# Kernel optimization log

Hardware: AMD Instinct MI355X
Metric: run time of the kernel (lower is better)

The kernel has to match this reference:

```python
import jax, jax.numpy as jnp
import numpy as np

N = 100000
E = 1600000
G = 128


def _degrees(src, dst, n):
    ones = jnp.ones(src.shape[0], dtype=jnp.float32)
    deg_out = jax.ops.segment_sum(ones, src, num_segments=n)
    deg_in = jax.ops.segment_sum(ones, dst, num_segments=n)
    return jnp.maximum(deg_out, 1.0), jnp.maximum(deg_in, 1.0)


def gcn_conv(x, W, b, src, dst, norm_out, norm_in):
    # DGL GraphConv, norm='both': scale src by d_out^-1/2, sum over edges,
    # scale dst by d_in^-1/2, then linear. Weight applied first (out<=in) --
    # mathematically identical, cheaper gather.
    h = (x * norm_out[:, None]) @ W          # [N, out]
    m = h[src]                               # [E, out] gather
    agg = jax.ops.segment_sum(m, dst, num_segments=N)  # [N, out] scatter-add
    return agg * norm_in[:, None] + b


def setup_inputs() -> dict:
    key = jax.random.key(0)
    ks = jax.random.split(key, 8)
    x = jax.random.normal(ks[0], (N, 128), dtype=jnp.float32)
    W1 = jax.random.normal(ks[1], (128, 64), dtype=jnp.float32) * (1.0 / np.sqrt(128))
    b1 = jnp.zeros((64,), dtype=jnp.float32)
    W2 = jax.random.normal(ks[2], (64, 16), dtype=jnp.float32) * (1.0 / np.sqrt(64))
    b2 = jnp.zeros((16,), dtype=jnp.float32)
    src = jax.random.randint(ks[3], (E,), 0, N, dtype=jnp.int32)
    dst = jax.random.randint(ks[4], (E,), 0, N, dtype=jnp.int32)
    graph_ids = jnp.sort(jax.random.randint(ks[5], (N,), 0, G, dtype=jnp.int32))
    return {"x": x, "W1": W1, "b1": b1, "W2": W2, "b2": b2,
            "src": src, "dst": dst, "graph_ids": graph_ids}


def reference(x, W1, b1, W2, b2, src, dst, graph_ids):
    deg_out, deg_in = _degrees(src, dst, N)
    norm_out = jax.lax.rsqrt(deg_out)
    norm_in = jax.lax.rsqrt(deg_in)
    h = gcn_conv(x, W1, b1, src, dst, norm_out, norm_in)
    h = jax.nn.relu(h)
    # dropout(p=0.2) is identity in eval mode
    h = gcn_conv(h, W2, b2, src, dst, norm_out, norm_in)
    # dgl.mean_nodes: per-graph mean pooling
    sums = jax.ops.segment_sum(h, graph_ids, num_segments=G)      # [G, 16]
    counts = jax.ops.segment_sum(jnp.ones((N,), jnp.float32), graph_ids, num_segments=G)
    return sums / jnp.maximum(counts, 1.0)[:, None]
```

## Files before the change

kernel.cpp:

```cpp
#include <hip/hip_runtime.h>
#include <hip/hip_fp16.h>

#define N_NODES 100000
#define N_EDGES 1600000
#define N_GRAPHS 128
#define NBUCK 391
#define NBLK 512
#define NE4 (N_EDGES / 4)
#define CHUNK_E4 782
#define LDX 136

typedef unsigned long long u64;
typedef unsigned int u32;
typedef unsigned char u8;
typedef _Float16 f16;
typedef f16 half8 __attribute__((ext_vector_type(8)));
typedef f16 half4v __attribute__((ext_vector_type(4)));
typedef float floatx4 __attribute__((ext_vector_type(4)));

__global__ __launch_bounds__(256) void k_cnt(const int4* __restrict__ src4,
                                             const int4* __restrict__ dst4,
                                             int* __restrict__ counts_d,
                                             int* __restrict__ counts_s) {
  __shared__ int hd[NBUCK], hs[NBUCK];
  const int t = threadIdx.x, blk = blockIdx.x;
  for (int j = t; j < NBUCK; j += 256) { hd[j] = 0; hs[j] = 0; }
  __syncthreads();
  const int start = blk * CHUNK_E4;
  const int end = min(start + CHUNK_E4, NE4);
  for (int i = start + t; i < end; i += 256) {
    int4 d = dst4[i]; int4 s = src4[i];
    atomicAdd(&hd[d.x >> 8], 1); atomicAdd(&hd[d.y >> 8], 1);
    atomicAdd(&hd[d.z >> 8], 1); atomicAdd(&hd[d.w >> 8], 1);
    atomicAdd(&hs[s.x >> 8], 1); atomicAdd(&hs[s.y >> 8], 1);
    atomicAdd(&hs[s.z >> 8], 1); atomicAdd(&hs[s.w >> 8], 1);
  }
  __syncthreads();
  for (int j = t; j < NBUCK; j += 256) {
    counts_d[j * NBLK + blk] = hd[j];
    counts_s[j * NBLK + blk] = hs[j];
  }
}

__global__ __launch_bounds__(512) void k_scanA(int* __restrict__ counts_d,
                                               int* __restrict__ counts_s,
                                               int* __restrict__ totals_d,
                                               int* __restrict__ totals_s) {
  __shared__ int s[512];
  const int b = blockIdx.x, t = threadIdx.x;
  int v = counts_d[b * NBLK + t];
  s[t] = v;
  __syncthreads();
  for (int off = 1; off < 512; off <<= 1) {
    int a = (t >= off) ? s[t - off] : 0;
    __syncthreads(); s[t] += a; __syncthreads();
  }
  counts_d[b * NBLK + t] = s[t] - v;
  if (t == 511) totals_d[b] = s[t];
  __syncthreads();
  v = counts_s[b * NBLK + t];
  s[t] = v;
  __syncthreads();
  for (int off = 1; off < 512; off <<= 1) {
    int a = (t >= off) ? s[t - off] : 0;
    __syncthreads(); s[t] += a; __syncthreads();
  }
  counts_s[b * NBLK + t] = s[t] - v;
  if (t == 511) totals_s[b] = s[t];
}

__global__ __launch_bounds__(512) void k_scanB(const int* __restrict__ totals_d,
                                               const int* __restrict__ totals_s,
                                               int* __restrict__ boff_d,
                                               int* __restrict__ boff_s,
                                               int* __restrict__ row_ptr) {
  __shared__ int s[512];
  const int t = threadIdx.x;
  int v = (t < NBUCK) ? totals_d[t] : 0;
  s[t] = v;
  __syncthreads();
  for (int off = 1; off < 512; off <<= 1) {
    int a = (t >= off) ? s[t - off] : 0;
    __syncthreads(); s[t] += a; __syncthreads();
  }
  if (t < NBUCK) boff_d[t] = s[t] - v;
  if (t == 0) { boff_d[NBUCK] = N_EDGES; row_ptr[N_NODES] = N_EDGES; }
  __syncthreads();
  v = (t < NBUCK) ? totals_s[t] : 0;
  s[t] = v;
  __syncthreads();
  for (int off = 1; off < 512; off <<= 1) {
    int a = (t >= off) ? s[t - off] : 0;
    __syncthreads(); s[t] += a; __syncthreads();
  }
  if (t < NBUCK) boff_s[t] = s[t] - v;
  if (t == 0) boff_s[NBUCK] = N_EDGES;
}

__global__ __launch_bounds__(256) void k_scatter(const int4* __restrict__ src4,
                                                 const int4* __restrict__ dst4,
                                                 const int* __restrict__ counts_d,
                                                 const int* __restrict__ counts_s,
                                                 const int* __restrict__ boff_d,
                                                 const int* __restrict__ boff_s,
                                                 u32* __restrict__ ed,
                                                 u8* __restrict__ ssk8) {
  __shared__ int cur_d[NBUCK], cur_s[NBUCK];
  const int t = threadIdx.x, blk = blockIdx.x;
  for (int j = t; j < NBUCK; j += 256) {
    cur_d[j] = boff_d[j] + counts_d[j * NBLK + blk];
    cur_s[j] = boff_s[j] + counts_s[j * NBLK + blk];
  }
  __syncthreads();
  const int start = blk * CHUNK_E4;
  const int end = min(start + CHUNK_E4, NE4);
  for (int i = start + t; i < end; i += 256) {
    int4 d4 = dst4[i]; int4 s4 = src4[i];
    {
      int d = d4.x, s = s4.x;
      int pd = atomicAdd(&cur_d[d >> 8], 1);
      ed[pd] = ((u32)(d & 255) << 24) | (u32)s;
      int ps = atomicAdd(&cur_s[s >> 8], 1);
      ssk8[ps] = (u8)(s & 255);
    }
    {
      int d = d4.y, s = s4.y;
      int pd = atomicAdd(&cur_d[d >> 8], 1);
      ed[pd] = ((u32)(d & 255) << 24) | (u32)s;
      int ps = atomicAdd(&cur_s[s >> 8], 1);
      ssk8[ps] = (u8)(s & 255);
    }
    {
      int d = d4.z, s = s4.z;
      int pd = atomicAdd(&cur_d[d >> 8], 1);
      ed[pd] = ((u32)(d & 255) << 24) | (u32)s;
      int ps = atomicAdd(&cur_s[s >> 8], 1);
      ssk8[ps] = (u8)(s & 255);
    }
    {
      int d = d4.w, s = s4.w;
      int pd = atomicAdd(&cur_d[d >> 8], 1);
      ed[pd] = ((u32)(d & 255) << 24) | (u32)s;
      int ps = atomicAdd(&cur_s[s >> 8], 1);
      ssk8[ps] = (u8)(s & 255);
    }
  }
}

__global__ __launch_bounds__(256) void k_bucket_csr(const u32* __restrict__ ed,
                                                    const int* __restrict__ boff_d,
                                                    const u8* __restrict__ ssk8,
                                                    const int* __restrict__ boff_s,
                                                    int* __restrict__ row_ptr,
                                                    float* __restrict__ norm_in,
                                                    float* __restrict__ norm_out,
                                                    int* __restrict__ edge_src) {
  __shared__ int hist[256], scanbuf[256], cursor[256], hist2[256];
  const int b = blockIdx.x, t = threadIdx.x;
  const int base = b << 8;
  hist[t] = 0; hist2[t] = 0;
  __syncthreads();
  const int slo = boff_s[b], shi = boff_s[b + 1];
  for (int i = slo + t; i < shi; i += 256)
    atomicAdd(&hist2[ssk8[i]], 1);
  const int lo = boff_d[b], hi = boff_d[b + 1];
  for (int i = lo + t; i < hi; i += 256)
    atomicAdd(&hist[ed[i] >> 24], 1);
  __syncthreads();
  int node = base + t;
  if (node < N_NODES)
    norm_out[node] = rsqrtf(fmaxf((float)hist2[t], 1.0f));
  int v = hist[t];
  scanbuf[t] = v;
  __syncthreads();
  for (int off = 1; off < 256; off <<= 1) {
    int a = (t >= off) ? scanbuf[t - off] : 0;
    __syncthreads(); scanbuf[t] += a; __syncthreads();
  }
  int excl = scanbuf[t] - v;
  if (node < N_NODES) {
    row_ptr[node] = lo + excl;
    norm_in[node] = rsqrtf(fmaxf((float)v, 1.0f));
  }
  cursor[t] = excl;
  __syncthreads();
  for (int i = lo + t; i < hi; i += 256) {
    u32 e = ed[i];
    int p = atomicAdd(&cursor[e >> 24], 1);
    edge_src[lo + p] = (int)(e & 0x00FFFFFFu);
  }
}

__global__ __launch_bounds__(256) void k_gemm1(const float* __restrict__ x,
                                               const float* __restrict__ W1,
                                               const float* __restrict__ norm_out,
                                               __half* __restrict__ h1h) {
  __shared__ __align__(16) f16 Xs[64 * LDX];
  __shared__ __align__(16) f16 Ws[64 * LDX];
  const int t = threadIdx.x;
  const int row0 = blockIdx.x * 64;

  const float4* W4 = (const float4*)W1;
  for (int i = t; i < 2048; i += 256) {
    int k = i >> 4, n4 = (i & 15) * 4;
    float4 v = W4[i];
    Ws[(n4 + 0) * LDX + k] = (f16)v.x;
    Ws[(n4 + 1) * LDX + k] = (f16)v.y;
    Ws[(n4 + 2) * LDX + k] = (f16)v.z;
    Ws[(n4 + 3) * LDX + k] = (f16)v.w;
  }
  const float4* x4 = (const float4*)x;
  #pragma unroll
  for (int i = 0; i < 8; ++i) {
    int idx = t + 256 * i;
    int r = idx >> 5, c4 = idx & 31;
    int row = row0 + r;
    float4 v = make_float4(0.f, 0.f, 0.f, 0.f);
    if (row < N_NODES) {
      float s = norm_out[row];
      v = x4[(size_t)row * 32 + c4];
      v.x *= s; v.y *= s; v.z *= s; v.w *= s;
    }
    half4v h = { (f16)v.x, (f16)v.y, (f16)v.z, (f16)v.w };
    *(half4v*)&Xs[r * LDX + c4 * 4] = h;
  }
  __syncthreads();

  const int w = t >> 6, l = t & 63;
  const int m = l & 15, quad = l >> 4;
  floatx4 c0 = {0.f,0.f,0.f,0.f}, c1 = {0.f,0.f,0.f,0.f};
  floatx4 c2 = {0.f,0.f,0.f,0.f}, c3 = {0.f,0.f,0.f,0.f};
  const f16* xrow = &Xs[(w * 16 + m) * LDX + quad * 8];
  const f16* wrow = &Ws[m * LDX + quad * 8];
  #pragma unroll
  for (int kb = 0; kb < 4; ++kb) {
    half8 a  = *(const half8*)(xrow + kb * 32);
    half8 b0 = *(const half8*)(wrow + kb * 32);
    half8 b1 = *(const half8*)(wrow + 16 * LDX + kb * 32);
    half8 b2 = *(const half8*)(wrow + 32 * LDX + kb * 32);
    half8 b3 = *(const half8*)(wrow + 48 * LDX + kb * 32);
    c0 = __builtin_amdgcn_mfma_f32_16x16x32_f16(a, b0, c0, 0, 0, 0);
    c1 = __builtin_amdgcn_mfma_f32_16x16x32_f16(a, b1, c1, 0, 0, 0);
    c2 = __builtin_amdgcn_mfma_f32_16x16x32_f16(a, b2, c2, 0, 0, 0);
    c3 = __builtin_amdgcn_mfma_f32_16x16x32_f16(a, b3, c3, 0, 0, 0);
  }
  #pragma unroll
  for (int r = 0; r < 4; ++r) {
    int row = row0 + w * 16 + quad * 4 + r;
    if (row < N_NODES + 1) {
      __half* dst = h1h + (size_t)row * 64 + m;
      dst[0]  = __float2half(c0[r]);
      dst[16] = __float2half(c1[r]);
      dst[32] = __float2half(c2[r]);
      dst[48] = __float2half(c3[r]);
    }
  }
}

__global__ __launch_bounds__(256) void k_gather_l1(const int* __restrict__ row_ptr,
                                                   const int* __restrict__ edge_src,
                                                   const __half* __restrict__ h1h,
                                                   const float* __restrict__ norm_in,
                                                   const float* __restrict__ norm_out,
                                                   const float* __restrict__ b1,
                                                   const float* __restrict__ W2,
                                                   __half* __restrict__ h2h) {
  __shared__ float W2s[64 * 17];
  const int t = threadIdx.x;
  for (int i = t; i < 64 * 16; i += 256) W2s[(i >> 4) * 17 + (i & 15)] = W2[i];
  if (blockIdx.x == 0 && t < 16) h2h[(size_t)N_NODES * 16 + t] = __float2half(0.f);
  __syncthreads();

  const int w = t >> 6;
  const int l = t & 63;
  const int n = blockIdx.x * 4 + w;
  const int p = l >> 3;
  const u32 c = (u32)(l & 7);

  const uint4* __restrict__ h1q = (const uint4*)h1h;
  const int lo = row_ptr[n], hi = row_ptr[n + 1];

  float2 f0 = {0.f,0.f}, f1 = {0.f,0.f}, f2 = {0.f,0.f}, f3 = {0.f,0.f};
  for (int i = lo; i < hi; i += 16) {
    int idx = i + (l & 15);
    int sv = (idx < hi) ? edge_src[idx] : (int)N_NODES;
    int sa = __shfl(sv, p, 64);
    int sb = __shfl(sv, p + 8, 64);
    uint4 va = h1q[(u32)sa * 8u + c];
    uint4 vb = h1q[(u32)sb * 8u + c];
    float2 g;
    g = __half22float2(*(__half2*)&va.x); f0.x += g.x; f0.y += g.y;
    g = __half22float2(*(__half2*)&va.y); f1.x += g.x; f1.y += g.y;
    g = __half22float2(*(__half2*)&va.z); f2.x += g.x; f2.y += g.y;
    g = __half22float2(*(__half2*)&va.w); f3.x += g.x; f3.y += g.y;
    g = __half22float2(*(__half2*)&vb.x); f0.x += g.x; f0.y += g.y;
    g = __half22float2(*(__half2*)&vb.y); f1.x += g.x; f1.y += g.y;
    g = __half22float2(*(__half2*)&vb.z); f2.x += g.x; f2.y += g.y;
    g = __half22float2(*(__half2*)&vb.w); f3.x += g.x; f3.y += g.y;
  }
  float hr[8] = { f0.x, f0.y, f1.x, f1.y, f2.x, f2.y, f3.x, f3.y };
  #pragma unroll
  for (int e = 0; e < 8; ++e) {
    hr[e] += __shfl_xor(hr[e], 8, 64);
    hr[e] += __shfl_xor(hr[e], 16, 64);
    hr[e] += __shfl_xor(hr[e], 32, 64);
  }
  const float ni = norm_in[n];
  const float4 bA = ((const float4*)b1)[c * 2];
  const float4 bB = ((const float4*)b1)[c * 2 + 1];
  hr[0] = fmaxf(hr[0] * ni + bA.x, 0.f);
  hr[1] = fmaxf(hr[1] * ni + bA.y, 0.f);
  hr[2] = fmaxf(hr[2] * ni + bA.z, 0.f);
  hr[3] = fmaxf(hr[3] * ni + bA.w, 0.f);
  hr[4] = fmaxf(hr[4] * ni + bB.x, 0.f);
  hr[5] = fmaxf(hr[5] * ni + bB.y, 0.f);
  hr[6] = fmaxf(hr[6] * ni + bB.z, 0.f);
  hr[7] = fmaxf(hr[7] * ni + bB.w, 0.f);

  const int j = l & 15, p2 = l >> 4;
  float partial = 0.f;
  #pragma unroll
  for (int e = 0; e < 8; ++e) {
    float v0 = __shfl(hr[e], p2 * 2, 64);
    float v1 = __shfl(hr[e], p2 * 2 + 1, 64);
    partial += v0 * W2s[(p2 * 16 + e) * 17 + j];
    partial += v1 * W2s[(p2 * 16 + 8 + e) * 17 + j];
  }
  partial += __shfl_xor(partial, 16, 64);
  partial += __shfl_xor(partial, 32, 64);
  if (l < 16) h2h[(size_t)n * 16 + l] = __float2half(norm_out[n] * partial);
}

__global__ __launch_bounds__(256) void k_gather_l2(const int* __restrict__ row_ptr,
                                                   const int* __restrict__ edge_src,
                                                   const __half* __restrict__ h2h,
                                                   const float* __restrict__ norm_in,
                                                   float* __restrict__ agg2) {
  const int t = threadIdx.x;
  const int w = t >> 6;
  const int l = t & 63;
  const int n = blockIdx.x * 4 + w;
  const int f2 = l & 7;
  const int p = l >> 3;

  const u32* __restrict__ h2u = (const u32*)h2h;
  const int lo = row_ptr[n], hi = row_ptr[n + 1];

  float ax = 0.f, ay = 0.f, bx = 0.f, by = 0.f;
  for (int base = lo; base < hi; base += 16) {
    int i1 = base + p, i2 = base + p + 8;
    int s0 = (i1 < hi) ? edge_src[i1] : (int)N_NODES;
    int s1 = (i2 < hi) ? edge_src[i2] : (int)N_NODES;
    u32 v0 = h2u[(u32)s0 * 8u + (u32)f2];
    u32 v1 = h2u[(u32)s1 * 8u + (u32)f2];
    float2 g0 = __half22float2(*(__half2*)&v0);
    float2 g1 = __half22float2(*(__half2*)&v1);
    ax += g0.x; ay += g0.y;
    bx += g1.x; by += g1.y;
  }
  float sx = ax + bx, sy = ay + by;
  sx += __shfl_xor(sx, 8, 64);  sy += __shfl_xor(sy, 8, 64);
  sx += __shfl_xor(sx, 16, 64); sy += __shfl_xor(sy, 16, 64);
  sx += __shfl_xor(sx, 32, 64); sy += __shfl_xor(sy, 32, 64);
  if (l < 8) {
    float ni = norm_in[n];
    ((float2*)agg2)[(size_t)n * 8 + f2] = make_float2(sx * ni, sy * ni);
  }
}

__global__ __launch_bounds__(256) void k_pool(const float* __restrict__ agg2,
                                              const float* __restrict__ b2,
                                              const int* __restrict__ gid,
                                              float* __restrict__ out) {
  const int g = blockIdx.x;
  __shared__ int s_lo, s_hi;
  if (threadIdx.x == 0) {
    int a = 0, b = N_NODES;
    while (a < b) { int m = (a + b) >> 1; if (gid[m] < g) a = m + 1; else b = m; }
    s_lo = a;
    b = N_NODES;
    while (a < b) { int m = (a + b) >> 1; if (gid[m] < g + 1) a = m + 1; else b = m; }
    s_hi = a;
  }
  __syncthreads();
  const int lo = s_lo, hi = s_hi, cnt = hi - lo;
  const int j = threadIdx.x & 15;
  const int r = threadIdx.x >> 4;
  float acc = 0.f;
  for (int n = lo + r; n < hi; n += 16)
    acc += agg2[(size_t)n * 16 + j];

  __shared__ float red[256];
  red[threadIdx.x] = acc;
  __syncthreads();
  #pragma unroll
  for (int s = 8; s > 0; s >>= 1) {
    if (r < s) red[threadIdx.x] += red[threadIdx.x + s * 16];
    __syncthreads();
  }
  if (r == 0)
    out[g * 16 + j] = (cnt > 0) ? (red[j] / (float)cnt + b2[j]) : 0.0f;
}

extern "C" void kernel_launch(void* const* d_in, const int* in_sizes, int n_in,
                              void* d_out, int out_size, void* d_ws, size_t ws_size,
                              hipStream_t stream) {
  const float* x   = (const float*)d_in[0];
  const float* W1  = (const float*)d_in[1];
  const float* b1  = (const float*)d_in[2];
  const float* W2  = (const float*)d_in[3];
  const float* b2  = (const float*)d_in[4];
  const int*   src = (const int*)d_in[5];
  const int*   dst = (const int*)d_in[6];
  const int*   gid = (const int*)d_in[7];
  float* out = (float*)d_out;

  const size_t N = N_NODES, E = N_EDGES;
  float* wsf = (float*)d_ws;
  int*   wsi = (int*)d_ws;

  float* norm_out = wsf;
  float* norm_in  = wsf + N;
  int*   row_ptr  = wsi + 2 * N;
  int*   edge_src = wsi + 3 * N + 16;
  size_t S = 3 * N + 16 + E;
  u8*    ssk8     = (u8*)(wsi + S);
  int*   counts_d = wsi + S + 400000;
  int*   counts_s = wsi + S + 600192;
  int*   totals_d = wsi + S + 800384;
  int*   totals_s = wsi + S + 800776;
  int*   boff_d   = wsi + S + 801168;
  int*   boff_s   = wsi + S + 801560;
  u32*   ed       = (u32*)(wsi + S + 801952);
  __half* h1h     = (__half*)(wsi + S);
  __half* h2h     = (__half*)(wsi + S + 32 * N + 32);
  float*  agg2    = (float*)(wsi + S + 40 * N + 40);

  const int4* src4 = (const int4*)src;
  const int4* dst4 = (const int4*)dst;

  k_cnt       <<<NBLK, 256, 0, stream>>>(src4, dst4, counts_d, counts_s);
  k_scanA     <<<NBUCK, 512, 0, stream>>>(counts_d, counts_s, totals_d, totals_s);
  k_scanB     <<<1, 512, 0, stream>>>(totals_d, totals_s, boff_d, boff_s, row_ptr);
  k_scatter   <<<NBLK, 256, 0, stream>>>(src4, dst4, counts_d, counts_s, boff_d, boff_s, ed, ssk8);
  k_bucket_csr<<<NBUCK, 256, 0, stream>>>(ed, boff_d, ssk8, boff_s, row_ptr, norm_in, norm_out, edge_src);
  k_gemm1     <<<(N_NODES + 64) / 64, 256, 0, stream>>>(x, W1, norm_out, h1h);
  k_gather_l1 <<<N_NODES / 4, 256, 0, stream>>>(row_ptr, edge_src, h1h, norm_in, norm_out, b1, W2, h2h);
  k_gather_l2 <<<N_NODES / 4, 256, 0, stream>>>(row_ptr, edge_src, h2h, norm_in, agg2);
  k_pool      <<<N_GRAPHS, 256, 0, stream>>>(agg2, b2, gid, out);
}
```

Measured before the change: 295.2 us.

## Replace per-node CSR with two-pass bucket sort and shared-memory atomic aggregation

The per-node CSR build is replaced by a two-pass radix-style sort: edges are first bucketed by source (for locality), then by destination into buckets of 64 nodes. The gather kernels now process one 64-node bucket per block and accumulate features with shared-memory float atomics instead of computing per-node row pointers. The two scans merge their second level via a last-block flag, which drops a launch. This aims to cut the cost of building the CSR and improve gather locality, but it adds heavy LDS atomic traffic and an extra pass over 8-byte edge records.

Measured after the change: 1.028 ms. 3.48x slower.

```diff
diff --git a/kernel.cpp b/kernel.cpp
--- a/kernel.cpp
+++ b/kernel.cpp
@@ -4,10 +4,12 @@
 #define N_NODES 100000
 #define N_EDGES 1600000
 #define N_GRAPHS 128
-#define NBUCK 391
+#define SB 391
+#define DB 1563
 #define NBLK 512
 #define NE4 (N_EDGES / 4)
-#define CHUNK_E4 782
+#define CH4 782
+#define CH64 3125
 #define LDX 136
 
 typedef unsigned long long u64;
@@ -18,176 +20,184 @@
 typedef f16 half4v __attribute__((ext_vector_type(4)));
 typedef float floatx4 __attribute__((ext_vector_type(4)));
 
-__global__ __launch_bounds__(256) void k_cnt(const int4* __restrict__ src4,
-                                             const int4* __restrict__ dst4,
-                                             int* __restrict__ counts_d,
-                                             int* __restrict__ counts_s) {
-  __shared__ int hd[NBUCK], hs[NBUCK];
-  const int t = threadIdx.x, blk = blockIdx.x;
-  for (int j = t; j < NBUCK; j += 256) { hd[j] = 0; hs[j] = 0; }
-  __syncthreads();
-  const int start = blk * CHUNK_E4;
-  const int end = min(start + CHUNK_E4, NE4);
+__global__ __launch_bounds__(256) void k_cnt_s(const int4* __restrict__ src4,
+                                               int* __restrict__ cs, int* __restrict__ flags) {
+  __shared__ int h[SB];
+  const int t = threadIdx.x, b = blockIdx.x;
+  if (b == 0 && t < 16) flags[t] = 0;
+  for (int j = t; j < SB; j += 256) h[j] = 0;
+  __syncthreads();
+  const int start = b * CH4, end = min(start + CH4, NE4);
   for (int i = start + t; i < end; i += 256) {
-    int4 d = dst4[i]; int4 s = src4[i];
-    atomicAdd(&hd[d.x >> 8], 1); atomicAdd(&hd[d.y >> 8], 1);
-    atomicAdd(&hd[d.z >> 8], 1); atomicAdd(&hd[d.w >> 8], 1);
-    atomicAdd(&hs[s.x >> 8], 1); atomicAdd(&hs[s.y >> 8], 1);
-    atomicAdd(&hs[s.z >> 8], 1); atomicAdd(&hs[s.w >> 8], 1);
-  }
-  __syncthreads();
-  for (int j = t; j < NBUCK; j += 256) {
-    counts_d[j * NBLK + blk] = hd[j];
-    counts_s[j * NBLK + blk] = hs[j];
-  }
-}
-
-__global__ __launch_bounds__(512) void k_scanA(int* __restrict__ counts_d,
-                                               int* __restrict__ counts_s,
-                                               int* __restrict__ totals_d,
-                                               int* __restrict__ totals_s) {
+    int4 s = src4[i];
+    atomicAdd(&h[s.x >> 8], 1); atomicAdd(&h[s.y >> 8], 1);
+    atomicAdd(&h[s.z >> 8], 1); atomicAdd(&h[s.w >> 8], 1);
+  }
+  __syncthreads();
+  for (int j = t; j < SB; j += 256) cs[j * NBLK + b] = h[j];
+}
+
+__global__ __launch_bounds__(512) void k_scan_s(int* __restrict__ cs, int* __restrict__ ts,
+                                                int* __restrict__ boff_s, int* __restrict__ flags) {
   __shared__ int s[512];
+  __shared__ int lastflag;
   const int b = blockIdx.x, t = threadIdx.x;
-  int v = counts_d[b * NBLK + t];
+  int v = cs[b * NBLK + t];
   s[t] = v;
   __syncthreads();
-  for (int off = 1; off < 512; off <<= 1) {
-    int a = (t >= off) ? s[t - off] : 0;
+  for (int o = 1; o < 512; o <<= 1) {
+    int a = (t >= o) ? s[t - o] : 0;
     __syncthreads(); s[t] += a; __syncthreads();
   }
-  counts_d[b * NBLK + t] = s[t] - v;
-  if (t == 511) totals_d[b] = s[t];
-  __syncthreads();
-  v = counts_s[b * NBLK + t];
+  cs[b * NBLK + t] = s[t] - v;
+  if (t == 511) atomicExch(&ts[b], s[t]);
+  if (t == 0) { __threadfence(); lastflag = (atomicAdd(&flags[0], 1) == SB - 1); }
+  __syncthreads();
+  if (!lastflag) return;
+  int v2 = (t < SB) ? atomicAdd(&ts[t], 0) : 0;
+  s[t] = v2;
+  __syncthreads();
+  for (int o = 1; o < 512; o <<= 1) {
+    int a = (t >= o) ? s[t - o] : 0;
+    __syncthreads(); s[t] += a; __syncthreads();
+  }
+  if (t <= SB) boff_s[t] = s[t] - v2;
+}
+
+__global__ __launch_bounds__(256) void k_scatter_s(const int4* __restrict__ src4,
+                                                   const int4* __restrict__ dst4,
+                                                   const int* __restrict__ cs,
+                                                   const int* __restrict__ boff_s,
+                                                   u64* __restrict__ ed_s, u8* __restrict__ ssk8) {
+  __shared__ int cur[SB];
+  const int t = threadIdx.x, b = blockIdx.x;
+  for (int j = t; j < SB; j += 256) cur[j] = boff_s[j] + cs[j * NBLK + b];
+  __syncthreads();
+  const int start = b * CH4, end = min(start + CH4, NE4);
+  for (int i = start + t; i < end; i += 256) {
+    int4 s4 = src4[i]; int4 d4 = dst4[i];
+    {
+      int s = s4.x, d = d4.x;
+      int ps = atomicAdd(&cur[s >> 8], 1);
+      ed_s[ps] = ((u64)(u32)d << 32) | (u32)s;
+      ssk8[ps] = (u8)(s & 255);
+    }
+    {
+      int s = s4.y, d = d4.y;
+      int ps = atomicAdd(&cur[s >> 8], 1);
+      ed_s[ps] = ((u64)(u32)d << 32) | (u32)s;
+      ssk8[ps] = (u8)(s & 255);
+    }
+    {
+      int s = s4.z, d = d4.z;
+      int ps = atomicAdd(&cur[s >> 8], 1);
+      ed_s[ps] = ((u64)(u32)d << 32) | (u32)s;
+      ssk8[ps] = (u8)(s & 255);
+    }
+    {
+      int s = s4.w, d = d4.w;
+      int ps = atomicAdd(&cur[s >> 8], 1);
+      ed_s[ps] = ((u64)(u32)d << 32) | (u32)s;
+      ssk8[ps] = (u8)(s & 255);
+    }
+  }
+}
+
+__global__ __launch_bounds__(256) void k_cnt_d(const u64* __restrict__ ed_s,
+                                               int* __restrict__ cd) {
+  __shared__ int h[DB];
+  const int t = threadIdx.x, b = blockIdx.x;
+  for (int j = t; j < DB; j += 256) h[j] = 0;
+  __syncthreads();
+  const int start = b * CH64, end = start + CH64;
+  for (int i = start + t; i < end; i += 256) {
+    u32 d = (u32)(ed_s[i] >> 32);
+    atomicAdd(&h[d >> 6], 1);
+  }
+  __syncthreads();
+  for (int j = t; j < DB; j += 256) cd[j * NBLK + b] = h[j];
+}
+
+__global__ __launch_bounds__(512) void k_scan_d(int* __restrict__ cd, int* __restrict__ td,
+                                                int* __restrict__ boff_d, int* __restrict__ flags) {
+  __shared__ int s[512];
+  __shared__ int lastflag;
+  const int b = blockIdx.x, t = threadIdx.x;
+  int v = cd[b * NBLK + t];
   s[t] = v;
   __syncthreads();
-  for (int off = 1; off < 512; off <<= 1) {
-    int a = (t >= off) ? s[t - off] : 0;
+  for (int o = 1; o < 512; o <<= 1) {
+    int a = (t >= o) ? s[t - o] : 0;
     __syncthreads(); s[t] += a; __syncthreads();
   }
-  counts_s[b * NBLK + t] = s[t] - v;
-  if (t == 511) totals_s[b] = s[t];
-}
-
-__global__ __launch_bounds__(512) void k_scanB(const int* __restrict__ totals_d,
-                                               const int* __restrict__ totals_s,
-                                               int* __restrict__ boff_d,
-                                               int* __restrict__ boff_s,
-                                               int* __restrict__ row_ptr) {
-  __shared__ int s[512];
-  const int t = threadIdx.x;
-  int v = (t < NBUCK) ? totals_d[t] : 0;
-  s[t] = v;
-  __syncthreads();
-  for (int off = 1; off < 512; off <<= 1) {
-    int a = (t >= off) ? s[t - off] : 0;
+  cd[b * NBLK + t] = s[t] - v;
+  if (t == 511) atomicExch(&td[b], s[t]);
+  if (t == 0) { __threadfence(); lastflag = (atomicAdd(&flags[1], 1) == DB - 1); }
+  __syncthreads();
+  if (!lastflag) return;
+  const int g = t * 4;
+  int v0 = (g + 0 < DB) ? atomicAdd(&td[g + 0], 0) : 0;
+  int v1 = (g + 1 < DB) ? atomicAdd(&td[g + 1], 0) : 0;
+  int v2 = (g + 2 < DB) ? atomicAdd(&td[g + 2], 0) : 0;
+  int v3 = (g + 3 < DB) ? atomicAdd(&td[g + 3], 0) : 0;
+  int tsum = v0 + v1 + v2 + v3;
+  s[t] = tsum;
+  __syncthreads();
+  for (int o = 1; o < 512; o <<= 1) {
+    int a = (t >= o) ? s[t - o] : 0;
     __syncthreads(); s[t] += a; __syncthreads();
   }
-  if (t < NBUCK) boff_d[t] = s[t] - v;
-  if (t == 0) { boff_d[NBUCK] = N_EDGES; row_ptr[N_NODES] = N_EDGES; }
-  __syncthreads();
-  v = (t < NBUCK) ? totals_s[t] : 0;
-  s[t] = v;
-  __syncthreads();
-  for (int off = 1; off < 512; off <<= 1) {
-    int a = (t >= off) ? s[t - off] : 0;
-    __syncthreads(); s[t] += a; __syncthreads();
-  }
-  if (t < NBUCK) boff_s[t] = s[t] - v;
-  if (t == 0) boff_s[NBUCK] = N_EDGES;
-}
-
-__global__ __launch_bounds__(256) void k_scatter(const int4* __restrict__ src4,
-                                                 const int4* __restrict__ dst4,
-                                                 const int* __restrict__ counts_d,
-                                                 const int* __restrict__ counts_s,
-                                                 const int* __restrict__ boff_d,
-                                                 const int* __restrict__ boff_s,
-                                                 u32* __restrict__ ed,
-                                                 u8* __restrict__ ssk8) {
-  __shared__ int cur_d[NBUCK], cur_s[NBUCK];
-  const int t = threadIdx.x, blk = blockIdx.x;
-  for (int j = t; j < NBUCK; j += 256) {
-    cur_d[j] = boff_d[j] + counts_d[j * NBLK + blk];
-    cur_s[j] = boff_s[j] + counts_s[j * NBLK + blk];
-  }
-  __syncthreads();
-  const int start = blk * CHUNK_E4;
-  const int end = min(start + CHUNK_E4, NE4);
+  int excl = s[t] - tsum;
+  if (g + 0 <= DB) boff_d[g + 0] = excl;
+  if (g + 1 <= DB) boff_d[g + 1] = excl + v0;
+  if (g + 2 <= DB) boff_d[g + 2] = excl + v0 + v1;
+  if (g + 3 <= DB) boff_d[g + 3] = excl + v0 + v1 + v2;
+}
+
+__global__ __launch_bounds__(256) void k_scatter_d(const u64* __restrict__ ed_s,
+                                                   const int* __restrict__ cd,
+                                                   const int* __restrict__ boff_d,
+                                                   u32* __restrict__ ed_d) {
+  __shared__ int cur[DB];
+  const int t = threadIdx.x, b = blockIdx.x;
+  for (int j = t; j < DB; j += 256) cur[j] = boff_d[j] + cd[j * NBLK + b];
+  __syncthreads();
+  const int start = b * CH64, end = start + CH64;
   for (int i = start + t; i < end; i += 256) {
-    int4 d4 = dst4[i]; int4 s4 = src4[i];
-    {
-      int d = d4.x, s = s4.x;
-      int pd = atomicAdd(&cur_d[d >> 8], 1);
-      ed[pd] = ((u32)(d & 255) << 24) | (u32)s;
-      int ps = atomicAdd(&cur_s[s >> 8], 1);
-      ssk8[ps] = (u8)(s & 255);
-    }
-    {
-      int d = d4.y, s = s4.y;
-      int pd = atomicAdd(&cur_d[d >> 8], 1);
-      ed[pd] = ((u32)(d & 255) << 24) | (u32)s;
-      int ps = atomicAdd(&cur_s[s >> 8], 1);
-      ssk8[ps] = (u8)(s & 255);
-    }
-    {
-      int d = d4.z, s = s4.z;
-      int pd = atomicAdd(&cur_d[d >> 8], 1);
-      ed[pd] = ((u32)(d & 255) << 24) | (u32)s;
-      int ps = atomicAdd(&cur_s[s >> 8], 1);
-      ssk8[ps] = (u8)(s & 255);
-    }
-    {
-      int d = d4.w, s = s4.w;
-      int pd = atomicAdd(&cur_d[d >> 8], 1);
-      ed[pd] = ((u32)(d & 255) << 24) | (u32)s;
-      int ps = atomicAdd(&cur_s[s >> 8], 1);
-      ssk8[ps] = (u8)(s & 255);
-    }
-  }
-}
-
-__global__ __launch_bounds__(256) void k_bucket_csr(const u32* __restrict__ ed,
-                                                    const int* __restrict__ boff_d,
-                                                    const u8* __restrict__ ssk8,
-                                                    const int* __restrict__ boff_s,
-                                                    int* __restrict__ row_ptr,
-                                                    float* __restrict__ norm_in,
-                                                    float* __restrict__ norm_out,
-                                                    int* __restrict__ edge_src) {
-  __shared__ int hist[256], scanbuf[256], cursor[256], hist2[256];
+    u64 e = ed_s[i];
+    u32 d = (u32)(e >> 32), s = (u32)e;
+    int pd = atomicAdd(&cur[d >> 6], 1);
+    ed_d[pd] = ((d & 63u) << 26) | s;
+  }
+}
+
+__global__ __launch_bounds__(256) void k_norms(const u8* __restrict__ ssk8,
+                                               const int* __restrict__ boff_s,
+                                               const u32* __restrict__ ed_d,
+                                               const int* __restrict__ boff_d,
+                                               float* __restrict__ norm_out,
+                                               float* __restrict__ norm_in) {
+  __shared__ int h[256];
   const int b = blockIdx.x, t = threadIdx.x;
-  const int base = b << 8;
-  hist[t] = 0; hist2[t] = 0;
-  __syncthreads();
-  const int slo = boff_s[b], shi = boff_s[b + 1];
-  for (int i = slo + t; i < shi; i += 256)
-    atomicAdd(&hist2[ssk8[i]], 1);
-  const int lo = boff_d[b], hi = boff_d[b + 1];
-  for (int i = lo + t; i < hi; i += 256)
-    atomicAdd(&hist[ed[i] >> 24], 1);
-  __syncthreads();
-  int node = base + t;
-  if (node < N_NODES)
-    norm_out[node] = rsqrtf(fmaxf((float)hist2[t], 1.0f));
-  int v = hist[t];
-  scanbuf[t] = v;
-  __syncthreads();
-  for (int off = 1; off < 256; off <<= 1) {
-    int a = (t >= off) ? scanbuf[t - off] : 0;
-    __syncthreads(); scanbuf[t] += a; __syncthreads();
-  }
-  int excl = scanbuf[t] - v;
-  if (node < N_NODES) {
-    row_ptr[node] = lo + excl;
-    norm_in[node] = rsqrtf(fmaxf((float)v, 1.0f));
-  }
-  cursor[t] = excl;
-  __syncthreads();
-  for (int i = lo + t; i < hi; i += 256) {
-    u32 e = ed[i];
-    int p = atomicAdd(&cursor[e >> 24], 1);
-    edge_src[lo + p] = (int)(e & 0x00FFFFFFu);
+  if (b < SB) {
+    h[t] = 0;
+    __syncthreads();
+    const int lo = boff_s[b], hi = boff_s[b + 1];
+    for (int i = lo + t; i < hi; i += 256) atomicAdd(&h[ssk8[i]], 1);
+    __syncthreads();
+    int node = (b << 8) + t;
+    if (node < N_NODES) norm_out[node] = rsqrtf(fmaxf((float)h[t], 1.0f));
+  } else {
+    const int bb = b - SB;
+    if (t < 64) h[t] = 0;
+    __syncthreads();
+    const int lo = boff_d[bb], hi = boff_d[bb + 1];
+    for (int i = lo + t; i < hi; i += 256) atomicAdd(&h[ed_d[i] >> 26], 1);
+    __syncthreads();
+    if (t < 64) {
+      int node = (bb << 6) + t;
+      if (node < N_NODES) norm_in[node] = rsqrtf(fmaxf((float)h[t], 1.0f));
+    }
   }
 }
 
@@ -257,114 +267,117 @@
   }
 }
 
-__global__ __launch_bounds__(256) void k_gather_l1(const int* __restrict__ row_ptr,
-                                                   const int* __restrict__ edge_src,
+__global__ __launch_bounds__(256) void k_gather_l1(const int* __restrict__ boff_d,
+                                                   const u32* __restrict__ ed_d,
                                                    const __half* __restrict__ h1h,
                                                    const float* __restrict__ norm_in,
                                                    const float* __restrict__ norm_out,
                                                    const float* __restrict__ b1,
                                                    const float* __restrict__ W2,
                                                    __half* __restrict__ h2h) {
-  __shared__ float W2s[64 * 17];
-  const int t = threadIdx.x;
-  for (int i = t; i < 64 * 16; i += 256) W2s[(i >> 4) * 17 + (i & 15)] = W2[i];
-  if (blockIdx.x == 0 && t < 16) h2h[(size_t)N_NODES * 16 + t] = __float2half(0.f);
-  __syncthreads();
-
-  const int w = t >> 6;
-  const int l = t & 63;
-  const int n = blockIdx.x * 4 + w;
-  const int p = l >> 3;
-  const u32 c = (u32)(l & 7);
-
+  __shared__ float acc[64 * 68];
+  __shared__ float W2s[64 * 16];
+  __shared__ float b1s[64];
+  const int t = threadIdx.x, b = blockIdx.x;
+  for (int i = t; i < 64 * 68; i += 256) acc[i] = 0.f;
+  for (int i = t; i < 1024; i += 256) W2s[i] = W2[i];
+  if (t < 64) b1s[t] = b1[t];
+  __syncthreads();
+
+  const int lo = boff_d[b], hi = boff_d[b + 1];
+  const int w = t >> 6, l = t & 63;
+  const int es = l >> 3;
+  const u32 q = (u32)(l & 7);
   const uint4* __restrict__ h1q = (const uint4*)h1h;
-  const int lo = row_ptr[n], hi = row_ptr[n + 1];
-
-  float2 f0 = {0.f,0.f}, f1 = {0.f,0.f}, f2 = {0.f,0.f}, f3 = {0.f,0.f};
-  for (int i = lo; i < hi; i += 16) {
-    int idx = i + (l & 15);
-    int sv = (idx < hi) ? edge_src[idx] : (int)N_NODES;
-    int sa = __shfl(sv, p, 64);
-    int sb = __shfl(sv, p + 8, 64);
-    uint4 va = h1q[(u32)sa * 8u + c];
-    uint4 vb = h1q[(u32)sb * 8u + c];
+
+  for (int i = lo + w * 16; i < hi; i += 64) {
+    int iA = i + es, iB = i + 8 + es;
+    u32 evA = (iA < hi) ? ed_d[iA] : (u32)N_NODES;
+    u32 evB = (iB < hi) ? ed_d[iB] : (u32)N_NODES;
+    u32 sA = evA & 0x3FFFFFFu, dA = evA >> 26;
+    u32 sB = evB & 0x3FFFFFFu, dB = evB >> 26;
+    uint4 va = h1q[sA * 8u + q];
+    uint4 vb = h1q[sB * 8u + q];
+    u32 pA = dA * 68u + q * 8u;
+    u32 pB = dB * 68u + q * 8u;
     float2 g;
-    g = __half22float2(*(__half2*)&va.x); f0.x += g.x; f0.y += g.y;
-    g = __half22float2(*(__half2*)&va.y); f1.x += g.x; f1.y += g.y;
-    g = __half22float2(*(__half2*)&va.z); f2.x += g.x; f2.y += g.y;
-    g = __half22float2(*(__half2*)&va.w); f3.x += g.x; f3.y += g.y;
-    g = __half22float2(*(__half2*)&vb.x); f0.x += g.x; f0.y += g.y;
-    g = __half22float2(*(__half2*)&vb.y); f1.x += g.x; f1.y += g.y;
-    g = __half22float2(*(__half2*)&vb.z); f2.x += g.x; f2.y += g.y;
-    g = __half22float2(*(__half2*)&vb.w); f3.x += g.x; f3.y += g.y;
-  }
-  float hr[8] = { f0.x, f0.y, f1.x, f1.y, f2.x, f2.y, f3.x, f3.y };
-  #pragma unroll
-  for (int e = 0; e < 8; ++e) {
-    hr[e] += __shfl_xor(hr[e], 8, 64);
-    hr[e] += __shfl_xor(hr[e], 16, 64);
-    hr[e] += __shfl_xor(hr[e], 32, 64);
-  }
-  const float ni = norm_in[n];
-  const float4 bA = ((const float4*)b1)[c * 2];
-  const float4 bB = ((const float4*)b1)[c * 2 + 1];
-  hr[0] = fmaxf(hr[0] * ni + bA.x, 0.f);
-  hr[1] = fmaxf(hr[1] * ni + bA.y, 0.f);
-  hr[2] = fmaxf(hr[2] * ni + bA.z, 0.f);
-  hr[3] = fmaxf(hr[3] * ni + bA.w, 0.f);
-  hr[4] = fmaxf(hr[4] * ni + bB.x, 0.f);
-  hr[5] = fmaxf(hr[5] * ni + bB.y, 0.f);
-  hr[6] = fmaxf(hr[6] * ni + bB.z, 0.f);
-  hr[7] = fmaxf(hr[7] * ni + bB.w, 0.f);
-
-  const int j = l & 15, p2 = l >> 4;
-  float partial = 0.f;
-  #pragma unroll
-  for (int e = 0; e < 8; ++e) {
-    float v0 = __shfl(hr[e], p2 * 2, 64);
-    float v1 = __shfl(hr[e], p2 * 2 + 1, 64);
-    partial += v0 * W2s[(p2 * 16 + e) * 17 + j];
-    partial += v1 * W2s[(p2 * 16 + 8 + e) * 17 + j];
-  }
-  partial += __shfl_xor(partial, 16, 64);
-  partial += __shfl_xor(partial, 32, 64);
-  if (l < 16) h2h[(size_t)n * 16 + l] = __float2half(norm_out[n] * partial);
-}
-
-__global__ __launch_bounds__(256) void k_gather_l2(const int* __restrict__ row_ptr,
-                                                   const int* __restrict__ edge_src,
+    g = __half22float2(*(__half2*)&va.x); atomicAdd(&acc[pA + 0], g.x); atomicAdd(&acc[pA + 1], g.y);
+    g = __half22float2(*(__half2*)&va.y); atomicAdd(&acc[pA + 2], g.x); atomicAdd(&acc[pA + 3], g.y);
+    g = __half22float2(*(__half2*)&va.z); atomicAdd(&acc[pA + 4], g.x); atomicAdd(&acc[pA + 5], g.y);
+    g = __half22float2(*(__half2*)&va.w); atomicAdd(&acc[pA + 6], g.x); atomicAdd(&acc[pA + 7], g.y);
+    g = __half22float2(*(__half2*)&vb.x); atomicAdd(&acc[pB + 0], g.x); atomicAdd(&acc[pB + 1], g.y);
+    g = __half22float2(*(__half2*)&vb.y); atomicAdd(&acc[pB + 2], g.x); atomicAdd(&acc[pB + 3], g.y);
+    g = __half22float2(*(__half2*)&vb.z); atomicAdd(&acc[pB + 4], g.x); atomicAdd(&acc[pB + 5], g.y);
+    g = __half22float2(*(__half2*)&vb.w); atomicAdd(&acc[pB + 6], g.x); atomicAdd(&acc[pB + 7], g.y);
+  }
+  __syncthreads();
+
+  const int nl = t >> 2, jg = t & 3;
+  const int node = (b << 6) + nl;
+  if (node <= N_NODES) {
+    float ni = (node < N_NODES) ? norm_in[node] : 0.f;
+    float no = (node < N_NODES) ? norm_out[node] : 0.f;
+    float o0 = 0.f, o1 = 0.f, o2 = 0.f, o3 = 0.f;
+    #pragma unroll
+    for (int k = 0; k < 64; k += 4) {
+      float4 r = *(float4*)&acc[nl * 68 + k];
+      float h0 = fmaxf(r.x * ni + b1s[k + 0], 0.f);
+      float h1v = fmaxf(r.y * ni + b1s[k + 1], 0.f);
+      float h2v = fmaxf(r.z * ni + b1s[k + 2], 0.f);
+      float h3v = fmaxf(r.w * ni + b1s[k + 3], 0.f);
+      int j = jg * 4;
+      o0 += h0 * W2s[(k + 0) * 16 + j + 0] + h1v * W2s[(k + 1) * 16 + j + 0]
+          + h2v * W2s[(k + 2) * 16 + j + 0] + h3v * W2s[(k + 3) * 16 + j + 0];
+      o1 += h0 * W2s[(k + 0) * 16 + j + 1] + h1v * W2s[(k + 1) * 16 + j + 1]
+          + h2v * W2s[(k + 2) * 16 + j + 1] + h3v * W2s[(k + 3) * 16 + j + 1];
+      o2 += h0 * W2s[(k + 0) * 16 + j + 2] + h1v * W2s[(k + 1) * 16 + j + 2]
+          + h2v * W2s[(k + 2) * 16 + j + 2] + h3v * W2s[(k + 3) * 16 + j + 2];
+      o3 += h0 * W2s[(k + 0) * 16 + j + 3] + h1v * W2s[(k + 1) * 16 + j + 3]
+          + h2v * W2s[(k + 2) * 16 + j + 3] + h3v * W2s[(k + 3) * 16 + j + 3];
+    }
+    __half2 q0 = __float22half2_rn(make_float2(no * o0, no * o1));
+    __half2 q1 = __float22half2_rn(make_float2(no * o2, no * o3));
+    uint2 pk = make_uint2(*(u32*)&q0, *(u32*)&q1);
+    *(uint2*)(h2h + (size_t)node * 16 + jg * 4) = pk;
+  }
+}
+
+__global__ __launch_bounds__(256) void k_gather_l2(const int* __restrict__ boff_d,
+                                                   const u32* __restrict__ ed_d,
                                                    const __half* __restrict__ h2h,
                                                    const float* __restrict__ norm_in,
                                                    float* __restrict__ agg2) {
-  const int t = threadIdx.x;
-  const int w = t >> 6;
-  const int l = t & 63;
-  const int n = blockIdx.x * 4 + w;
-  const int f2 = l & 7;
-  const int p = l >> 3;
-
+  __shared__ float acc[64 * 20];
+  const int t = threadIdx.x, b = blockIdx.x;
+  for (int i = t; i < 64 * 20; i += 256) acc[i] = 0.f;
+  __syncthreads();
+
+  const int lo = boff_d[b], hi = boff_d[b + 1];
+  const int w = t >> 6, l = t & 63;
+  const int es = l >> 2;
+  const u32 q = (u32)(l & 3);
   const u32* __restrict__ h2u = (const u32*)h2h;
-  const int lo = row_ptr[n], hi = row_ptr[n + 1];
-
-  float ax = 0.f, ay = 0.f, bx = 0.f, by = 0.f;
-  for (int base = lo; base < hi; base += 16) {
-    int i1 = base + p, i2 = base + p + 8;
-    int s0 = (i1 < hi) ? edge_src[i1] : (int)N_NODES;
-    int s1 = (i2 < hi) ? edge_src[i2] : (int)N_NODES;
-    u32 v0 = h2u[(u32)s0 * 8u + (u32)f2];
-    u32 v1 = h2u[(u32)s1 * 8u + (u32)f2];
-    float2 g0 = __half22float2(*(__half2*)&v0);
-    float2 g1 = __half22float2(*(__half2*)&v1);
-    ax += g0.x; ay += g0.y;
-    bx += g1.x; by += g1.y;
-  }
-  float sx = ax + bx, sy = ay + by;
-  sx += __shfl_xor(sx, 8, 64);  sy += __shfl_xor(sy, 8, 64);
-  sx += __shfl_xor(sx, 16, 64); sy += __shfl_xor(sy, 16, 64);
-  sx += __shfl_xor(sx, 32, 64); sy += __shfl_xor(sy, 32, 64);
-  if (l < 8) {
-    float ni = norm_in[n];
-    ((float2*)agg2)[(size_t)n * 8 + f2] = make_float2(sx * ni, sy * ni);
+
+  for (int i = lo + w * 16; i < hi; i += 64) {
+    int idx = i + es;
+    u32 ev = (idx < hi) ? ed_d[idx] : (u32)N_NODES;
+    u32 s = ev & 0x3FFFFFFu, dl = ev >> 26;
+    uint2 v = *(const uint2*)(h2u + s * 8u + q * 2u);
+    float2 g0 = __half22float2(*(__half2*)&v.x);
+    float2 g1 = __half22float2(*(__half2*)&v.y);
+    u32 p = dl * 20u + q * 4u;
+    atomicAdd(&acc[p + 0], g0.x); atomicAdd(&acc[p + 1], g0.y);
+    atomicAdd(&acc[p + 2], g1.x); atomicAdd(&acc[p + 3], g1.y);
+  }
+  __syncthreads();
+
+  const int nl = t >> 2, qq = t & 3;
+  const int node = (b << 6) + nl;
+  if (node < N_NODES) {
+    float ni = norm_in[node];
+    float4 r = *(float4*)&acc[nl * 20 + qq * 4];
+    *(float4*)(agg2 + (size_t)node * 16 + qq * 4) =
+        make_float4(r.x * ni, r.y * ni, r.z * ni, r.w * ni);
   }
 }
 
@@ -415,37 +428,37 @@
   const int*   gid = (const int*)d_in[7];
   float* out = (float*)d_out;
 
-  const size_t N = N_NODES, E = N_EDGES;
+  int* wsi = (int*)d_ws;
   float* wsf = (float*)d_ws;
-  int*   wsi = (int*)d_ws;
-
-  float* norm_out = wsf;
-  float* norm_in  = wsf + N;
-  int*   row_ptr  = wsi + 2 * N;
-  int*   edge_src = wsi + 3 * N + 16;
-  size_t S = 3 * N + 16 + E;
-  u8*    ssk8     = (u8*)(wsi + S);
-  int*   counts_d = wsi + S + 400000;
-  int*   counts_s = wsi + S + 600192;
-  int*   totals_d = wsi + S + 800384;
-  int*   totals_s = wsi + S + 800776;
-  int*   boff_d   = wsi + S + 801168;
-  int*   boff_s   = wsi + S + 801560;
-  u32*   ed       = (u32*)(wsi + S + 801952);
-  __half* h1h     = (__half*)(wsi + S);
-  __half* h2h     = (__half*)(wsi + S + 32 * N + 32);
-  float*  agg2    = (float*)(wsi + S + 40 * N + 40);
+
+  float* norm_out = wsf + 0;
+  float* norm_in  = wsf + 100000;
+  int*   ts       = wsi + 200000;
+  int*   td       = wsi + 200400;
+  int*   boff_s   = wsi + 202000;
+  int*   boff_d   = wsi + 202400;
+  int*   flags    = wsi + 204000;
+  int*   cs       = wsi + 204016;
+  int*   cd       = wsi + 404208;
+  u8*    ssk8     = (u8*)(wsi + 1204464);
+  u32*   ed_d     = (u32*)(wsi + 1604464);
+  u64*   ed_s     = (u64*)(wsi + 3204464);
+  __half* h1h     = (__half*)(wsi + 3204464);
+  __half* h2h     = (__half*)(wsi + 404208);
+  float*  agg2    = (float*)(wsi + 3204464);
 
   const int4* src4 = (const int4*)src;
   const int4* dst4 = (const int4*)dst;
 
-  k_cnt       <<<NBLK, 256, 0, stream>>>(src4, dst4, counts_d, counts_s);
-  k_scanA     <<<NBUCK, 512, 0, stream>>>(counts_d, counts_s, totals_d, totals_s);
-  k_scanB     <<<1, 512, 0, stream>>>(totals_d, totals_s, boff_d, boff_s, row_ptr);
-  k_scatter   <<<NBLK, 256, 0, stream>>>(src4, dst4, counts_d, counts_s, boff_d, boff_s, ed, ssk8);
-  k_bucket_csr<<<NBUCK, 256, 0, stream>>>(ed, boff_d, ssk8, boff_s, row_ptr, norm_in, norm_out, edge_src);
+  k_cnt_s     <<<NBLK, 256, 0, stream>>>(src4, cs, flags);
+  k_scan_s    <<<SB, 512, 0, stream>>>(cs, ts, boff_s, flags);
+  k_scatter_s <<<NBLK, 256, 0, stream>>>(src4, dst4, cs, boff_s, ed_s, ssk8);
+  k_cnt_d     <<<NBLK, 256, 0, stream>>>(ed_s, cd);
+  k_scan_d    <<<DB, 512, 0, stream>>>(cd, td, boff_d, flags);
+  k_scatter_d <<<NBLK, 256, 0, stream>>>(ed_s, cd, boff_d, ed_d);
+  k_norms     <<<SB + DB, 256, 0, stream>>>(ssk8, boff_s, ed_d, boff_d, norm_out, norm_in);
   k_gemm1     <<<(N_NODES + 64) / 64, 256, 0, stream>>>(x, W1, norm_out, h1h);
-  k_gather_l1 <<<N_NODES / 4, 256, 0, stream>>>(row_ptr, edge_src, h1h, norm_in, norm_out, b1, W2, h2h);
-  k_gather_l2 <<<N_NODES / 4, 256, 0, stream>>>(row_ptr, edge_src, h2h, norm_in, agg2);
+  k_gather_l1 <<<DB, 256, 0, stream>>>(boff_d, ed_d, h1h, norm_in, norm_out, b1, W2, h2h);
+  k_gather_l2 <<<DB, 256, 0, stream>>>(boff_d, ed_d, h2h, norm_in, agg2);
   k_pool      <<<N_GRAPHS, 256, 0, stream>>>(agg2, b2, gid, out);
 }
```
